# Performance work log

Hardware: AMD Instinct MI355X
Metric: run time of the kernel (lower is better)

Reference implementation:

```python
import jax, jax.numpy as jnp
import numpy as np

B, T, C, H, W = 8, 10, 1, 64, 64
HID = 64

def conv2d_same(x, w):
    return jax.lax.conv_general_dilated(x, w, (1, 1), 'SAME', dimension_numbers=('NCHW', 'OIHW', 'NCHW'))

def setup_inputs():
    key = jax.random.key(0)
    ks = iter(jax.random.split(key, 32))
    inp = {'x': jax.random.uniform(next(ks), (B, T, C, H, W), jnp.float32)}
    def cell_params(prefix, in_ch):
        # 4 gates (i, f, g, o) stacked along output channels -> fused gate conv
        inp[prefix + '_Wx'] = jax.random.normal(next(ks), (4 * HID, in_ch, 3, 3), jnp.float32) * 0.05
        inp[prefix + '_Wh'] = jax.random.normal(next(ks), (4 * HID, HID, 3, 3), jnp.float32) * 0.05
        inp[prefix + '_Wc'] = jax.random.normal(next(ks), (4, HID, H, W), jnp.float32) * 0.05
        inp[prefix + '_b'] = jax.random.normal(next(ks), (4, HID, H, W), jnp.float32) * 0.05
    cell_params('enc0', C)
    cell_params('enc1', HID)
    cell_params('dec0', HID)
    cell_params('dec1', HID)
    inp['fin_w'] = jax.random.normal(next(ks), (1, HID, 3, 3), jnp.float32) * 0.05
    inp['fin_b'] = jnp.zeros((1,), jnp.float32)
    inp['prediction_len'] = 10
    return inp

def _cell(Wx, Wh, Wc, b, xt, h, c):
    # gate = act(W_x*x + W_h*h + W_c.c + bias); all 4 gates use the OLD (h, c)
    hid = h.shape[1]
    pre = conv2d_same(xt, Wx) + conv2d_same(h, Wh)  # (B, 4*hid, H, W)
    pre = pre.reshape(pre.shape[0], 4, hid, pre.shape[2], pre.shape[3])
    pre = pre + Wc[None] * c[:, None] + b[None]
    i = jax.nn.sigmoid(pre[:, 0])
    f = jax.nn.sigmoid(pre[:, 1])
    g = jnp.tanh(pre[:, 2])
    o = jax.nn.sigmoid(pre[:, 3])
    c_new = f * c + i * g
    h_new = o * jnp.tanh(c_new)
    return h_new, c_new

def reference(x, enc0_Wx, enc0_Wh, enc0_Wc, enc0_b, enc1_Wx, enc1_Wh, enc1_Wc, enc1_b, dec0_Wx, dec0_Wh, dec0_Wc, dec0_b, dec1_Wx, dec1_Wh, dec1_Wc, dec1_b, fin_w, fin_b, prediction_len):
    b_, t_ = x.shape[0], x.shape[1]
    h_, w_ = x.shape[3], x.shape[4]
    hid = enc0_Wc.shape[1]
    z = jnp.zeros((b_, hid, h_, w_), x.dtype)

    def enc_step(carry, xt):
        h0, c0, h1, c1 = carry
        h0, c0 = _cell(enc0_Wx, enc0_Wh, enc0_Wc, enc0_b, xt, h0, c0)
        h1, c1 = _cell(enc1_Wx, enc1_Wh, enc1_Wc, enc1_b, h0, h1, c1)
        return (h0, c0, h1, c1), None

    (eh0, ec0, eh1, ec1), _ = jax.lax.scan(enc_step, (z, z, z, z), jnp.swapaxes(x, 0, 1))
    state = eh1  # top-layer encoder hidden; decoder h/c start at zeros (as in torch code)

    def dec_step(carry, _):
        s, h0, c0, h1, c1 = carry
        h0, c0 = _cell(dec0_Wx, dec0_Wh, dec0_Wc, dec0_b, s, h0, c0)
        h1, c1 = _cell(dec1_Wx, dec1_Wh, dec1_Wc, dec1_b, h0, h1, c1)
        return (h1, h0, c0, h1, c1), h1

    _, ys = jax.lax.scan(dec_step, (state, z, z, z, z), None, length=prediction_len)
    # ys: (F, B, hid, H, W); Conv3d with (1,3,3) kernel == per-frame 2d conv
    f_ = ys.shape[0]
    y = ys.reshape(f_ * b_, hid, h_, w_)
    y = conv2d_same(y, fin_w) + fin_b[None, :, None, None]
    y = y.reshape(f_, b_, 1, h_, w_)
    return jax.nn.sigmoid(jnp.swapaxes(y, 0, 1))  # (B, F, 1, H, W)
```

## Files before the change

### kernel.cpp

```cpp
#include <hip/hip_runtime.h>
#include <hip/hip_bf16.h>
#include <math.h>

#define BSZ    8
#define TSTEPS 10
#define FLEN   10
#define HID    64
#define HW     4096
#define IMG    (HID * HW)
#define OC4    (4 * HID)
#define PADW   66
#define PADIMG (PADW * PADW * HID)
#define PADSZ  (BSZ * PADIMG)
#define SB     (BSZ * IMG)
#define KT_E0  640
#define KT_STD 1152

typedef __attribute__((ext_vector_type(8))) short bf16x8;
typedef __attribute__((ext_vector_type(4))) float f32x4;

__device__ __forceinline__ float sigmoidf_(float x) {
    return 1.0f / (1.0f + __expf(-x));
}
__device__ __forceinline__ float tanh_fast(float x) {
    float e = __expf(2.0f * x);
    return 1.0f - 2.0f / (e + 1.0f);
}
__device__ __forceinline__ float bf2f(short u) {
    union { unsigned u; float f; } cv;
    cv.u = ((unsigned)(unsigned short)u) << 16;
    return cv.f;
}

__global__ __launch_bounds__(256) void reorder_w(
    const float* __restrict__ Wx, int icx,
    const float* __restrict__ Wh, __hip_bfloat16* __restrict__ Bw, int ktot) {
    int ocp = blockIdx.x, hid = ocp >> 2, gate = ocp & 3;
    int oc = gate * 64 + hid;
    for (int k = threadIdx.x; k < ktot; k += 256) {
        int c = k >> 6, j = k & 63;
        float v;
        if (icx == 1) {
            if (c == 0) v = (j < 9) ? Wx[oc * 9 + j] : 0.0f;
            else        v = Wh[(oc * 64 + j) * 9 + (c - 1)];
        } else {
            if (c < 9)  v = Wx[(oc * 64 + j) * 9 + c];
            else        v = Wh[(oc * 64 + j) * 9 + (c - 9)];
        }
        Bw[ocp * ktot + k] = __float2bfloat16(v);
    }
}

__global__ __launch_bounds__(256) void pack_x_all(
    const float* __restrict__ x, __hip_bfloat16* __restrict__ px_all) {
    int i = blockIdx.x * 256 + threadIdx.x;
    int t = i >> 15, rem = i & 32767;
    int b = rem >> 12, p = rem & 4095, y = p >> 6, xx = p & 63;
    const float* xb = x + ((size_t)(b * TSTEPS + t)) * HW;
    __hip_bfloat16* o = px_all + (size_t)t * PADSZ +
                        ((b * PADW + y + 1) * PADW + (xx + 1)) * HID;
#pragma unroll
    for (int tap = 0; tap < 9; tap++) {
        int yy = y + tap / 3 - 1, xc = xx + tap % 3 - 1;
        float v = (yy >= 0 && yy < 64 && xc >= 0 && xc < 64) ? xb[yy * 64 + xc] : 0.0f;
        o[tap] = __float2bfloat16(v);
    }
}

template <bool FIRST>
__global__ __launch_bounds__(256) void gemm_cell_fused(
    const __hip_bfloat16* __restrict__ Bw, int ktot, int n0,
    const __hip_bfloat16* __restrict__ src0,
    const __hip_bfloat16* __restrict__ src1,
    const float* __restrict__ Wc, const float* __restrict__ bias,
    float* __restrict__ cbuf, __hip_bfloat16* __restrict__ hout) {
    __shared__ short As[128 * 64];
    __shared__ short Bs[128 * 64];
    const int tid  = threadIdx.x;
    const int lane = tid & 63;
    const int wave = tid >> 6;
    const int quad = lane >> 4;
    const int l15  = lane & 15;
    const int wr = wave >> 1;
    const int wc = wave & 1;
    const int px0 = blockIdx.x * 128;
    const int oc0 = blockIdx.y * 128;

    int a_off[4], s_off[4];
#pragma unroll
    for (int it = 0; it < 4; it++) {
        int idx = it * 256 + tid;
        int rr = idx >> 3, seg = idx & 7;
        int segx = seg ^ (rr & 7);
        a_off[it] = (oc0 + rr) * ktot + segx * 8;
        int px = px0 + rr;
        int b = px >> 12, p = px & 4095, y = p >> 6, x = p & 63;
        s_off[it] = ((b * PADW + y + 1) * PADW + (x + 1)) * HID + segx * 8;
    }
    const int ldsbase = (tid & ~63) * 8;
    const int xa = l15 & 7;

    f32x4 acc[4][4] = {};
    const int nchunks = n0 + 9;

    for (int kk = 0; kk < nchunks; kk++) {
        const __hip_bfloat16* src;
        int tap;
        if (kk < n0) { src = src0; tap = (n0 == 1) ? 4 : kk; }
        else         { src = src1; tap = kk - n0; }
        int dd = ((tap / 3) - 1) * (PADW * HID) + ((tap % 3) - 1) * HID;
        int ka = kk * 64;
#pragma unroll
        for (int it = 0; it < 4; it++) {
            __builtin_amdgcn_global_load_lds(
                (const __attribute__((address_space(1))) void*)(Bw + a_off[it] + ka),
                (__attribute__((address_space(3))) void*)(&As[it * 2048 + ldsbase]),
                16, 0, 0);
            __builtin_amdgcn_global_load_lds(
                (const __attribute__((address_space(1))) void*)(src + s_off[it] + dd),
                (__attribute__((address_space(3))) void*)(&Bs[it * 2048 + ldsbase]),
                16, 0, 0);
        }
        __syncthreads();
#pragma unroll
        for (int k2 = 0; k2 < 2; k2++) {
            int sA = ((k2 * 4 + quad) ^ xa) * 8;
            bf16x8 af[4], bfr[4];
#pragma unroll
            for (int i = 0; i < 4; i++)
                af[i] = *(const bf16x8*)&As[(wr * 64 + i * 16 + l15) * 64 + sA];
#pragma unroll
            for (int j = 0; j < 4; j++)
                bfr[j] = *(const bf16x8*)&Bs[(wc * 64 + j * 16 + l15) * 64 + sA];
#pragma unroll
            for (int i = 0; i < 4; i++)
#pragma unroll
                for (int j = 0; j < 4; j++)
                    acc[i][j] = __builtin_amdgcn_mfma_f32_16x16x32_bf16(
                        af[i], bfr[j], acc[i][j], 0, 0, 0);
        }
        __syncthreads();
    }

#pragma unroll
    for (int i = 0; i < 4; i++) {
        int hid = (oc0 >> 2) + wr * 16 + i * 4 + quad;
#pragma unroll
        for (int j = 0; j < 4; j++) {
            int px = px0 + wc * 64 + j * 16 + l15;
            int b = px >> 12, p = px & 4095, y = p >> 6, x = p & 63;
            size_t ci = ((size_t)(b * HID + hid)) * HW + p;
            float cv = FIRST ? 0.0f : cbuf[ci];
            float pg[4];
#pragma unroll
            for (int r = 0; r < 4; r++) {
                int wi = (r * HID + hid) * HW + p;
                float t = acc[i][j][r] + bias[wi];
                if (!FIRST) t += Wc[wi] * cv;
                pg[r] = t;
            }
            float ig = sigmoidf_(pg[0]);
            float fg = sigmoidf_(pg[1]);
            float gg = tanh_fast(pg[2]);
            float og = sigmoidf_(pg[3]);
            float cn = FIRST ? (ig * gg) : (fg * cv + ig * gg);
            cbuf[ci] = cn;
            float hn = og * tanh_fast(cn);
            hout[((b * PADW + y + 1) * PADW + (x + 1)) * HID + hid] =
                __float2bfloat16(hn);
        }
    }
}

__global__ __launch_bounds__(256) void final_conv(
    const __hip_bfloat16* __restrict__ ph, const float* __restrict__ fw,
    const float* __restrict__ fb, float* __restrict__ out, int f) {
    int b = blockIdx.y;
    int p = blockIdx.x * 256 + threadIdx.x;
    int y = p >> 6, x = p & 63;
    float acc = fb[0];
#pragma unroll
    for (int tap = 0; tap < 9; tap++) {
        const bf16x8* base = (const bf16x8*)(
            ph + ((b * PADW + y + (tap / 3)) * PADW + (x + (tap % 3))) * HID);
#pragma unroll
        for (int c8 = 0; c8 < 8; c8++) {
            bf16x8 v = base[c8];
#pragma unroll
            for (int jj = 0; jj < 8; jj++)
                acc = fmaf(bf2f(v[jj]), fw[(c8 * 8 + jj) * 9 + tap], acc);
        }
    }
    out[((size_t)(b * FLEN + f)) * HW + p] = sigmoidf_(acc);
}

extern "C" void kernel_launch(void* const* d_in, const int* in_sizes, int n_in,
                              void* d_out, int out_size, void* d_ws, size_t ws_size,
                              hipStream_t stream) {
    const float* x = (const float*)d_in[0];
    const float* Wx_[4] = {(const float*)d_in[1], (const float*)d_in[5],
                           (const float*)d_in[9], (const float*)d_in[13]};
    const float* Wh_[4] = {(const float*)d_in[2], (const float*)d_in[6],
                           (const float*)d_in[10], (const float*)d_in[14]};
    const float* Wc_[4] = {(const float*)d_in[3], (const float*)d_in[7],
                           (const float*)d_in[11], (const float*)d_in[15]};
    const float* b_[4]  = {(const float*)d_in[4], (const float*)d_in[8],
                           (const float*)d_in[12], (const float*)d_in[16]};
    const float* fin_w  = (const float*)d_in[17];
    const float* fin_b  = (const float*)d_in[18];
    float* out = (float*)d_out;

    char* wsb = (char*)d_ws;
    const size_t PADS_BYTES = 18ull * PADSZ * sizeof(short);
    const size_t C_BYTES    = 4ull * SB * sizeof(float);

    __hip_bfloat16* pads = (__hip_bfloat16*)wsb;
    float* cbuf = (float*)(wsb + PADS_BYTES);
    __hip_bfloat16* bw = (__hip_bfloat16*)(wsb + PADS_BYTES + C_BYTES);

    __hip_bfloat16* px_all = pads;
    __hip_bfloat16* e0buf[2] = {pads + 10 * (size_t)PADSZ, pads + 11 * (size_t)PADSZ};
    __hip_bfloat16* e1buf[2] = {pads + 12 * (size_t)PADSZ, pads + 13 * (size_t)PADSZ};
    __hip_bfloat16* d0buf[2] = {pads + 14 * (size_t)PADSZ, pads + 15 * (size_t)PADSZ};
    __hip_bfloat16* d1buf[2] = {pads + 16 * (size_t)PADSZ, pads + 17 * (size_t)PADSZ};

    float* ec0 = cbuf + 0 * (size_t)SB;
    float* ec1 = cbuf + 1 * (size_t)SB;
    float* dc0 = cbuf + 2 * (size_t)SB;
    float* dc1 = cbuf + 3 * (size_t)SB;

    __hip_bfloat16* bw_e0 = bw;
    __hip_bfloat16* bw_e1 = bw_e0 + (size_t)OC4 * KT_E0;
    __hip_bfloat16* bw_d0 = bw_e1 + (size_t)OC4 * KT_STD;
    __hip_bfloat16* bw_d1 = bw_d0 + (size_t)OC4 * KT_STD;

    hipMemsetAsync(wsb, 0, PADS_BYTES, stream);

    reorder_w<<<dim3(OC4), 256, 0, stream>>>(Wx_[0], 1,   Wh_[0], bw_e0, KT_E0);
    reorder_w<<<dim3(OC4), 256, 0, stream>>>(Wx_[1], HID, Wh_[1], bw_e1, KT_STD);
    reorder_w<<<dim3(OC4), 256, 0, stream>>>(Wx_[2], HID, Wh_[2], bw_d0, KT_STD);
    reorder_w<<<dim3(OC4), 256, 0, stream>>>(Wx_[3], HID, Wh_[3], bw_d1, KT_STD);
    pack_x_all<<<dim3((TSTEPS * BSZ * HW) / 256), 256, 0, stream>>>(x, px_all);

    dim3 ggemm(256, 2);
    dim3 gfin(16, BSZ);

    int pp = 0;
    for (int t = 0; t < TSTEPS; t++) {
        const __hip_bfloat16* xt = px_all + (size_t)t * PADSZ;
        if (t == 0) {
            gemm_cell_fused<true><<<ggemm, 256, 0, stream>>>(
                bw_e0, KT_E0, 1, xt, e0buf[pp], Wc_[0], b_[0], ec0, e0buf[1 - pp]);
            gemm_cell_fused<true><<<ggemm, 256, 0, stream>>>(
                bw_e1, KT_STD, 9, e0buf[1 - pp], e1buf[pp], Wc_[1], b_[1], ec1, e1buf[1 - pp]);
        } else {
            gemm_cell_fused<false><<<ggemm, 256, 0, stream>>>(
                bw_e0, KT_E0, 1, xt, e0buf[pp], Wc_[0], b_[0], ec0, e0buf[1 - pp]);
            gemm_cell_fused<false><<<ggemm, 256, 0, stream>>>(
                bw_e1, KT_STD, 9, e0buf[1 - pp], e1buf[pp], Wc_[1], b_[1], ec1, e1buf[1 - pp]);
        }
        pp ^= 1;
    }
    __hip_bfloat16* enc_top = e1buf[0];

    int qq = 0;
    for (int f = 0; f < FLEN; f++) {
        const __hip_bfloat16* s = (f == 0) ? enc_top : d1buf[qq];
        if (f == 0) {
            gemm_cell_fused<true><<<ggemm, 256, 0, stream>>>(
                bw_d0, KT_STD, 9, s, d0buf[qq], Wc_[2], b_[2], dc0, d0buf[1 - qq]);
            gemm_cell_fused<true><<<ggemm, 256, 0, stream>>>(
                bw_d1, KT_STD, 9, d0buf[1 - qq], d1buf[qq], Wc_[3], b_[3], dc1, d1buf[1 - qq]);
        } else {
            gemm_cell_fused<false><<<ggemm, 256, 0, stream>>>(
                bw_d0, KT_STD, 9, s, d0buf[qq], Wc_[2], b_[2], dc0, d0buf[1 - qq]);
            gemm_cell_fused<false><<<ggemm, 256, 0, stream>>>(
                bw_d1, KT_STD, 9, d0buf[1 - qq], d1buf[qq], Wc_[3], b_[3], dc1, d1buf[1 - qq]);
        }
        final_conv<<<gfin, 256, 0, stream>>>(d1buf[1 - qq], fin_w, fin_b, out, f);
        qq ^= 1;
    }
}
```

Measured before the change: 1.569 ms.

## Wavefront-pipeline encoder cells, pack Wc/bias to bf16, and coalesce h stores via LDS

The encoder's layer-0 step t and layer-1 step t-1 now run in one launch, split across blockIdx.z, so the two cells run concurrently with fewer launches and better occupancy. Wc and bias are pre-packed into one interleaved bf16x8 per (hid, pixel), replacing eight strided fp32 loads in the epilogue with one vector load, at some precision cost. Hidden outputs are staged in LDS and written as 16-byte vectors instead of scattered 2-byte stores. pack_x_all now writes whole padded pixels, including the border, with vector stores, so the input region no longer needs a memset.

```diff
diff --git a/kernel.cpp b/kernel.cpp
--- a/kernel.cpp
+++ b/kernel.cpp
@@ -10,7 +10,8 @@
 #define IMG    (HID * HW)
 #define OC4    (4 * HID)
 #define PADW   66
-#define PADIMG (PADW * PADW * HID)
+#define PPIX   (PADW * PADW)
+#define PADIMG (PPIX * HID)
 #define PADSZ  (BSZ * PADIMG)
 #define SB     (BSZ * IMG)
 #define KT_E0  640
@@ -30,6 +31,11 @@
     union { unsigned u; float f; } cv;
     cv.u = ((unsigned)(unsigned short)u) << 16;
     return cv.f;
+}
+__device__ __forceinline__ short f2bf(float x) {
+    __hip_bfloat16 h = __float2bfloat16(x);
+    union { __hip_bfloat16 h; short s; } cv; cv.h = h;
+    return cv.s;
 }
 
 __global__ __launch_bounds__(256) void reorder_w(
@@ -51,31 +57,73 @@
     }
 }
 
+__global__ __launch_bounds__(256) void pack_wcb(
+    const float* __restrict__ Wc, const float* __restrict__ bias,
+    __hip_bfloat16* __restrict__ wcb) {
+    int i = blockIdx.x * 256 + threadIdx.x;
+    int hid = i >> 12, p = i & 4095;
+    union { short s[8]; bf16x8 v; } u;
+#pragma unroll
+    for (int g = 0; g < 4; g++) {
+        u.s[g]     = f2bf(Wc[(g * HID + hid) * HW + p]);
+        u.s[4 + g] = f2bf(bias[(g * HID + hid) * HW + p]);
+    }
+    *(bf16x8*)&wcb[(size_t)i * 8] = u.v;
+}
+
 __global__ __launch_bounds__(256) void pack_x_all(
     const float* __restrict__ x, __hip_bfloat16* __restrict__ px_all) {
     int i = blockIdx.x * 256 + threadIdx.x;
-    int t = i >> 15, rem = i & 32767;
-    int b = rem >> 12, p = rem & 4095, y = p >> 6, xx = p & 63;
+    if (i >= TSTEPS * BSZ * PPIX) return;
+    int t = i / (BSZ * PPIX);
+    int rem = i - t * (BSZ * PPIX);
+    int b = rem / PPIX;
+    int pp = rem - b * PPIX;
+    int y = pp / PADW, xx = pp - y * PADW;
+    int oy = y - 1, ox = xx - 1;
     const float* xb = x + ((size_t)(b * TSTEPS + t)) * HW;
-    __hip_bfloat16* o = px_all + (size_t)t * PADSZ +
-                        ((b * PADW + y + 1) * PADW + (xx + 1)) * HID;
+    bool interior = (oy >= 0 && oy < 64 && ox >= 0 && ox < 64);
+    union { short s[16]; bf16x8 v[2]; } u;
 #pragma unroll
     for (int tap = 0; tap < 9; tap++) {
-        int yy = y + tap / 3 - 1, xc = xx + tap % 3 - 1;
-        float v = (yy >= 0 && yy < 64 && xc >= 0 && xc < 64) ? xb[yy * 64 + xc] : 0.0f;
-        o[tap] = __float2bfloat16(v);
-    }
-}
-
-template <bool FIRST>
-__global__ __launch_bounds__(256) void gemm_cell_fused(
-    const __hip_bfloat16* __restrict__ Bw, int ktot, int n0,
-    const __hip_bfloat16* __restrict__ src0,
-    const __hip_bfloat16* __restrict__ src1,
-    const float* __restrict__ Wc, const float* __restrict__ bias,
-    float* __restrict__ cbuf, __hip_bfloat16* __restrict__ hout) {
+        int yy = oy + tap / 3 - 1, xc = ox + tap % 3 - 1;
+        float val = (interior && yy >= 0 && yy < 64 && xc >= 0 && xc < 64)
+                        ? xb[yy * 64 + xc] : 0.0f;
+        u.s[tap] = f2bf(val);
+    }
+#pragma unroll
+    for (int tap = 9; tap < 16; tap++) u.s[tap] = 0;
+    short* o = (short*)(px_all + (size_t)t * PADSZ + ((size_t)(b * PPIX + pp)) * HID);
+    *(bf16x8*)&o[0] = u.v[0];
+    *(bf16x8*)&o[8] = u.v[1];
+}
+
+struct CellArgs {
+    const __hip_bfloat16* Bw;
+    const __hip_bfloat16* src0;
+    const __hip_bfloat16* src1;
+    const __hip_bfloat16* wcb;
+    float* cbuf;
+    __hip_bfloat16* hout;
+    int ktot;
+    int n0;
+    int first;
+};
+
+__global__ __launch_bounds__(256) void gemm_cell_fused(CellArgs A0, CellArgs A1) {
     __shared__ short As[128 * 64];
     __shared__ short Bs[128 * 64];
+    const bool z1 = (blockIdx.z != 0);
+    const __hip_bfloat16* __restrict__ Bw   = z1 ? A1.Bw   : A0.Bw;
+    const __hip_bfloat16* __restrict__ src0 = z1 ? A1.src0 : A0.src0;
+    const __hip_bfloat16* __restrict__ src1 = z1 ? A1.src1 : A0.src1;
+    const __hip_bfloat16* __restrict__ wcb  = z1 ? A1.wcb  : A0.wcb;
+    float* __restrict__ cbuf                = z1 ? A1.cbuf : A0.cbuf;
+    __hip_bfloat16* __restrict__ hout       = z1 ? A1.hout : A0.hout;
+    const int ktot  = z1 ? A1.ktot  : A0.ktot;
+    const int n0    = z1 ? A1.n0    : A0.n0;
+    const int first = z1 ? A1.first : A0.first;
+
     const int tid  = threadIdx.x;
     const int lane = tid & 63;
     const int wave = tid >> 6;
@@ -142,33 +190,44 @@
         __syncthreads();
     }
 
+    short* hl = As;
+    const int hid0 = oc0 >> 2;
 #pragma unroll
     for (int i = 0; i < 4; i++) {
-        int hid = (oc0 >> 2) + wr * 16 + i * 4 + quad;
+        int hidl = wr * 16 + i * 4 + quad;
+        int hid = hid0 + hidl;
 #pragma unroll
         for (int j = 0; j < 4; j++) {
-            int px = px0 + wc * 64 + j * 16 + l15;
-            int b = px >> 12, p = px & 4095, y = p >> 6, x = p & 63;
+            int pxl = wc * 64 + j * 16 + l15;
+            int px = px0 + pxl;
+            int b = px >> 12, p = px & 4095;
             size_t ci = ((size_t)(b * HID + hid)) * HW + p;
-            float cv = FIRST ? 0.0f : cbuf[ci];
+            float cv = first ? 0.0f : cbuf[ci];
+            bf16x8 wv = *(const bf16x8*)&wcb[((size_t)hid * HW + p) * 8];
             float pg[4];
 #pragma unroll
-            for (int r = 0; r < 4; r++) {
-                int wi = (r * HID + hid) * HW + p;
-                float t = acc[i][j][r] + bias[wi];
-                if (!FIRST) t += Wc[wi] * cv;
-                pg[r] = t;
-            }
+            for (int r = 0; r < 4; r++)
+                pg[r] = acc[i][j][r] + bf2f(wv[r]) * cv + bf2f(wv[4 + r]);
             float ig = sigmoidf_(pg[0]);
             float fg = sigmoidf_(pg[1]);
             float gg = tanh_fast(pg[2]);
             float og = sigmoidf_(pg[3]);
-            float cn = FIRST ? (ig * gg) : (fg * cv + ig * gg);
+            float cn = fg * cv + ig * gg;
             cbuf[ci] = cn;
             float hn = og * tanh_fast(cn);
-            hout[((b * PADW + y + 1) * PADW + (x + 1)) * HID + hid] =
-                __float2bfloat16(hn);
-        }
+            hl[pxl * 40 + hidl] = f2bf(hn);
+        }
+    }
+    __syncthreads();
+#pragma unroll
+    for (int rnd = 0; rnd < 2; rnd++) {
+        int task = rnd * 256 + tid;
+        int pxl = task >> 2, q = task & 3;
+        bf16x8 v = *(const bf16x8*)&hl[pxl * 40 + q * 8];
+        int px = px0 + pxl;
+        int b = px >> 12, p = px & 4095, y = p >> 6, x = p & 63;
+        *(bf16x8*)&hout[((size_t)((b * PADW + y + 1) * PADW + (x + 1))) * HID
+                        + hid0 + q * 8] = v;
     }
 }
 
@@ -211,73 +270,82 @@
     float* out = (float*)d_out;
 
     char* wsb = (char*)d_ws;
-    const size_t PADS_BYTES = 18ull * PADSZ * sizeof(short);
-    const size_t C_BYTES    = 4ull * SB * sizeof(float);
-
-    __hip_bfloat16* pads = (__hip_bfloat16*)wsb;
-    float* cbuf = (float*)(wsb + PADS_BYTES);
-    __hip_bfloat16* bw = (__hip_bfloat16*)(wsb + PADS_BYTES + C_BYTES);
-
-    __hip_bfloat16* px_all = pads;
-    __hip_bfloat16* e0buf[2] = {pads + 10 * (size_t)PADSZ, pads + 11 * (size_t)PADSZ};
-    __hip_bfloat16* e1buf[2] = {pads + 12 * (size_t)PADSZ, pads + 13 * (size_t)PADSZ};
-    __hip_bfloat16* d0buf[2] = {pads + 14 * (size_t)PADSZ, pads + 15 * (size_t)PADSZ};
-    __hip_bfloat16* d1buf[2] = {pads + 16 * (size_t)PADSZ, pads + 17 * (size_t)PADSZ};
+    const size_t H_BYTES  = 8ull * PADSZ * sizeof(short);
+    const size_t PX_BYTES = 10ull * PADSZ * sizeof(short);
+    const size_t C_BYTES  = 4ull * SB * sizeof(float);
+    const size_t WCB_ELEM = (size_t)HID * HW * 8;
+
+    __hip_bfloat16* hb = (__hip_bfloat16*)wsb;
+    __hip_bfloat16* px_all = (__hip_bfloat16*)(wsb + H_BYTES);
+    float* cbuf = (float*)(wsb + H_BYTES + PX_BYTES);
+    __hip_bfloat16* wcb = (__hip_bfloat16*)(wsb + H_BYTES + PX_BYTES + C_BYTES);
+    __hip_bfloat16* bw = wcb + 4 * WCB_ELEM;
+
+    __hip_bfloat16* e0buf[2] = {hb + 0 * (size_t)PADSZ, hb + 1 * (size_t)PADSZ};
+    __hip_bfloat16* e1buf[2] = {hb + 2 * (size_t)PADSZ, hb + 3 * (size_t)PADSZ};
+    __hip_bfloat16* d0buf[2] = {hb + 4 * (size_t)PADSZ, hb + 5 * (size_t)PADSZ};
+    __hip_bfloat16* d1buf[2] = {hb + 6 * (size_t)PADSZ, hb + 7 * (size_t)PADSZ};
 
     float* ec0 = cbuf + 0 * (size_t)SB;
     float* ec1 = cbuf + 1 * (size_t)SB;
     float* dc0 = cbuf + 2 * (size_t)SB;
     float* dc1 = cbuf + 3 * (size_t)SB;
 
+    __hip_bfloat16* wcb_[4] = {wcb, wcb + WCB_ELEM, wcb + 2 * WCB_ELEM, wcb + 3 * WCB_ELEM};
     __hip_bfloat16* bw_e0 = bw;
     __hip_bfloat16* bw_e1 = bw_e0 + (size_t)OC4 * KT_E0;
     __hip_bfloat16* bw_d0 = bw_e1 + (size_t)OC4 * KT_STD;
     __hip_bfloat16* bw_d1 = bw_d0 + (size_t)OC4 * KT_STD;
-
-    hipMemsetAsync(wsb, 0, PADS_BYTES, stream);
+    __hip_bfloat16* bw_[4] = {bw_e0, bw_e1, bw_d0, bw_d1};
+    float* c_[4] = {ec0, ec1, dc0, dc1};
+
+    hipMemsetAsync(wsb, 0, H_BYTES, stream);
 
     reorder_w<<<dim3(OC4), 256, 0, stream>>>(Wx_[0], 1,   Wh_[0], bw_e0, KT_E0);
     reorder_w<<<dim3(OC4), 256, 0, stream>>>(Wx_[1], HID, Wh_[1], bw_e1, KT_STD);
     reorder_w<<<dim3(OC4), 256, 0, stream>>>(Wx_[2], HID, Wh_[2], bw_d0, KT_STD);
     reorder_w<<<dim3(OC4), 256, 0, stream>>>(Wx_[3], HID, Wh_[3], bw_d1, KT_STD);
-    pack_x_all<<<dim3((TSTEPS * BSZ * HW) / 256), 256, 0, stream>>>(x, px_all);
-
-    dim3 ggemm(256, 2);
+    for (int cix = 0; cix < 4; cix++)
+        pack_wcb<<<dim3((HID * HW) / 256), 256, 0, stream>>>(Wc_[cix], b_[cix], wcb_[cix]);
+    pack_x_all<<<dim3((TSTEPS * BSZ * PPIX + 255) / 256), 256, 0, stream>>>(x, px_all);
+
+    auto cellargs = [&](int cell, const __hip_bfloat16* s0, const __hip_bfloat16* s1,
+                        __hip_bfloat16* ho, int kt, int nn0, int fi) {
+        CellArgs a;
+        a.Bw = bw_[cell]; a.src0 = s0; a.src1 = s1; a.wcb = wcb_[cell];
+        a.cbuf = c_[cell]; a.hout = ho; a.ktot = kt; a.n0 = nn0; a.first = fi;
+        return a;
+    };
+    auto px = [&](int t) { return px_all + (size_t)t * PADSZ; };
+
     dim3 gfin(16, BSZ);
 
-    int pp = 0;
-    for (int t = 0; t < TSTEPS; t++) {
-        const __hip_bfloat16* xt = px_all + (size_t)t * PADSZ;
-        if (t == 0) {
-            gemm_cell_fused<true><<<ggemm, 256, 0, stream>>>(
-                bw_e0, KT_E0, 1, xt, e0buf[pp], Wc_[0], b_[0], ec0, e0buf[1 - pp]);
-            gemm_cell_fused<true><<<ggemm, 256, 0, stream>>>(
-                bw_e1, KT_STD, 9, e0buf[1 - pp], e1buf[pp], Wc_[1], b_[1], ec1, e1buf[1 - pp]);
-        } else {
-            gemm_cell_fused<false><<<ggemm, 256, 0, stream>>>(
-                bw_e0, KT_E0, 1, xt, e0buf[pp], Wc_[0], b_[0], ec0, e0buf[1 - pp]);
-            gemm_cell_fused<false><<<ggemm, 256, 0, stream>>>(
-                bw_e1, KT_STD, 9, e0buf[1 - pp], e1buf[pp], Wc_[1], b_[1], ec1, e1buf[1 - pp]);
-        }
-        pp ^= 1;
-    }
-    __hip_bfloat16* enc_top = e1buf[0];
-
-    int qq = 0;
+    {
+        CellArgs a = cellargs(0, px(0), e0buf[1], e0buf[0], KT_E0, 1, 1);
+        gemm_cell_fused<<<dim3(256, 2, 1), 256, 0, stream>>>(a, a);
+    }
+    for (int k = 1; k <= 9; k++) {
+        int t0 = k, t1 = k - 1;
+        CellArgs a0 = cellargs(0, px(t0), e0buf[(t0 - 1) & 1], e0buf[t0 & 1],
+                               KT_E0, 1, 0);
+        CellArgs a1 = cellargs(1, e0buf[t1 & 1], e1buf[(t1 - 1) & 1], e1buf[t1 & 1],
+                               KT_STD, 9, (t1 == 0) ? 1 : 0);
+        gemm_cell_fused<<<dim3(256, 2, 2), 256, 0, stream>>>(a0, a1);
+    }
+    {
+        CellArgs a = cellargs(1, e0buf[1], e1buf[0], e1buf[1], KT_STD, 9, 0);
+        gemm_cell_fused<<<dim3(256, 2, 1), 256, 0, stream>>>(a, a);
+    }
+    __hip_bfloat16* enc_top = e1buf[1];
+
     for (int f = 0; f < FLEN; f++) {
-        const __hip_bfloat16* s = (f == 0) ? enc_top : d1buf[qq];
-        if (f == 0) {
-            gemm_cell_fused<true><<<ggemm, 256, 0, stream>>>(
-                bw_d0, KT_STD, 9, s, d0buf[qq], Wc_[2], b_[2], dc0, d0buf[1 - qq]);
-            gemm_cell_fused<true><<<ggemm, 256, 0, stream>>>(
-                bw_d1, KT_STD, 9, d0buf[1 - qq], d1buf[qq], Wc_[3], b_[3], dc1, d1buf[1 - qq]);
-        } else {
-            gemm_cell_fused<false><<<ggemm, 256, 0, stream>>>(
-                bw_d0, KT_STD, 9, s, d0buf[qq], Wc_[2], b_[2], dc0, d0buf[1 - qq]);
-            gemm_cell_fused<false><<<ggemm, 256, 0, stream>>>(
-                bw_d1, KT_STD, 9, d0buf[1 - qq], d1buf[qq], Wc_[3], b_[3], dc1, d1buf[1 - qq]);
-        }
-        final_conv<<<gfin, 256, 0, stream>>>(d1buf[1 - qq], fin_w, fin_b, out, f);
-        qq ^= 1;
-    }
-}
+        const __hip_bfloat16* s = (f == 0) ? enc_top : d1buf[(f - 1) & 1];
+        CellArgs a0 = cellargs(2, s, d0buf[(f - 1) & 1], d0buf[f & 1],
+                               KT_STD, 9, (f == 0) ? 1 : 0);
+        gemm_cell_fused<<<dim3(256, 2, 1), 256, 0, stream>>>(a0, a0);
+        CellArgs a1 = cellargs(3, d0buf[f & 1], d1buf[(f - 1) & 1], d1buf[f & 1],
+                               KT_STD, 9, (f == 0) ? 1 : 0);
+        gemm_cell_fused<<<dim3(256, 2, 1), 256, 0, stream>>>(a1, a1);
+        final_conv<<<gfin, 256, 0, stream>>>(d1buf[f & 1], fin_w, fin_b, out, f);
+    }
+}
```

After: 1.567 ms. About the same (-0.1%).
